# Kernel optimization log

Measured on AMD Instinct MI355X. Metric: run time of the kernel, lower is better.

Reference implementation:

```python
import jax, jax.numpy as jnp
import numpy as np

TS = 1.0  # simulation time step (Ts from network.yaml)


def alpha_psp(x, tau):
    """SLAYER psp: causal temporal conv of x (time-major, (T,...)) with the
    SRM alpha kernel eps[k] = (k*Ts/tau)*exp(1 - k*Ts/tau), scaled by Ts.
    eps[k] = (Ts*e/tau) * k * d**k with d = exp(-Ts/tau), realized exactly by a
    2-state linear recurrence instead of an O(T^2) FIR."""
    d = jnp.asarray(np.exp(-TS / tau), x.dtype)
    c = jnp.asarray(np.e * TS / tau * TS, x.dtype)  # kernel amp * Ts integration

    def step(carry, x_t):
        u, v = carry                       # u = sum x_s d^(t-1-s); v = sum x_s (t-1-s) d^(t-1-s)
        v_new = d * (v + u)                # -> sum_{s<=t} x_s (t-s) d^(t-s)  (x_t weight 0)
        u_new = d * u + x_t
        return (u_new, v_new), c * v_new

    z = jnp.zeros_like(x[0])
    _, out = jax.lax.scan(step, (z, z), x)
    return out


def lif_spike(u_in, theta, tauRef, scaleRef):
    """SLAYER spike function: sequential threshold over time with alpha-shaped
    refractory response nu[k] = -scaleRef*theta*(k*Ts/tauRef)*exp(1-k*Ts/tauRef)
    added after every spike. Same 2-state recurrence generates the refractory
    sum exactly. u_in is time-major (T, ...). Spike amplitude is 1/Ts."""
    d = jnp.asarray(np.exp(-TS / tauRef), u_in.dtype)
    c = jnp.asarray(-scaleRef * theta * np.e * TS / tauRef, u_in.dtype)

    def step(carry, u_t):
        u, v = carry
        v_new = d * (v + u)                # refractory state from past spikes only
        m = u_t + c * v_new                # membrane potential incl. refractory
        s = (m >= theta).astype(u_t.dtype)
        return (d * u + s, v_new), (s / TS, m)

    z = jnp.zeros_like(u_in[0])
    _, (spikes, membrane) = jax.lax.scan(step, (z, z), u_in)
    return spikes, membrane


def conv2d_t(x, w, pad):
    """Per-time-step 2D conv (SLAYER conv3d with time-kernel 1, no bias).
    x: (T, N, C, H, W), w: (O, I, kh, kw)."""
    T, N, C, H, W = x.shape
    y = jax.lax.conv_general_dilated(
        x.reshape(T * N, C, H, W), w, (1, 1), [(pad, pad), (pad, pad)],
        dimension_numbers=('NCHW', 'OIHW', 'NCHW'))
    return y.reshape(T, N, -1, H, W)


def setup_inputs() -> dict:
    key = jax.random.key(0)
    k1, k2, k3 = jax.random.split(key, 3)
    # binary event spike train, (N, C, H, W, T)
    spikeInput = (jax.random.uniform(k1, (4, 1, 192, 192, 64)) < 0.2).astype(jnp.float32)
    # SLAYER conv weights (bias=False); scaled up (weightScale~100 in SLAYER)
    W1 = jax.random.normal(k2, (1, 1, 5, 5), jnp.float32) * 10.0
    W2 = jax.random.normal(k3, (1, 1, 3, 3), jnp.float32) * 10.0
    return {"spikeInput": spikeInput, "W1": W1, "W2": W2}


def reference(spikeInput, W1, W2):
    x = jnp.moveaxis(spikeInput, -1, 0)          # (T, N, C, H, W) time-major
    psp1 = alpha_psp(x, tau=1.0)                 # slayer1.psp (tauSr=1)
    s1, _ = lif_spike(conv2d_t(psp1, W1, 2), theta=30.0, tauRef=1.0, scaleRef=1.0)
    psp2 = alpha_psp(s1, tau=2.0)                # slayer2.psp (tauSr=2)
    s2, _ = lif_spike(conv2d_t(psp2, W2, 1), theta=50.0, tauRef=2.0, scaleRef=1.0)
    return jnp.moveaxis(s2, 0, -1)               # back to (N, C, H, W, T)
```

## Files before the change

### kernel.cpp

```cpp
#include <hip/hip_runtime.h>


#define HH   192
#define WW   192
#define NIMG 4
#define TT   64
#define NT   256
#define XW   6
#define XH   12

#define E_D 2.718281828459045
static constexpr float D1  = (float)0.36787944117144233;
static constexpr float CP1 = (float)(E_D);
static constexpr float DR1 = (float)0.36787944117144233;
static constexpr float CR1 = (float)(-30.0 * E_D);
static constexpr float D2  = (float)0.6065306597126334;
static constexpr float CP2 = (float)(E_D * 0.5);
static constexpr float DR2 = (float)0.6065306597126334;
static constexpr float CR2 = (float)(-50.0 * E_D * 0.5);
static constexpr float TH1 = 30.0f;
static constexpr float TH2 = 50.0f;

__global__ __launch_bounds__(NT)
void ka_pack(const float* __restrict__ in, unsigned* __restrict__ bitT) {
    const int gw = blockIdx.x * (NT / 64) + (threadIdx.x >> 6);
    const int ln = threadIdx.x & 63;
    const int xw = gw % XW;
    const int ny = gw / XW;
    const float* src = in + ((size_t)ny * WW + xw * 32) * TT + ln;
    unsigned w = 0u;
#pragma unroll
    for (int x = 0; x < 32; x++) {
        const float v = src[(size_t)x * TT];
        w |= (v != 0.f) ? (1u << x) : 0u;
    }
    bitT[((size_t)ny * XW + xw) * TT + ln] = w;
}

__global__ __launch_bounds__(NT, 8)
void l1_convscan(const unsigned* __restrict__ bitT, const float* __restrict__ w1g,
                 unsigned short* __restrict__ s1h) {
    __shared__ float ct[64 * 65];
    __shared__ uint2 tb[64];

    const int n = blockIdx.z, ys = blockIdx.y, xs = blockIdx.x;
    const int y0 = ys * 4, x0 = xs * 16;
    const int tid = threadIdx.x;
    const int wv = tid >> 6, ln = tid & 63;

    float w1r[25];
#pragma unroll
    for (int k = 0; k < 25; k++) w1r[k] = w1g[k];

    const int a = (x0 - 2) >> 5;
    const int s = (x0 - 2) & 31;
    const int gyb = y0 + wv;
    unsigned w20[5];
#pragma unroll
    for (int dy = 0; dy < 5; dy++) {
        const int gy = gyb - 2 + dy;
        unsigned wa = 0u, wb = 0u;
        if (gy >= 0 && gy < HH) {
            const unsigned* rp = bitT + ((size_t)(n * HH + gy) * XW) * TT + ln;
            if (a >= 0)     wa = rp[(size_t)a * TT];
            if (a + 1 < XW) wb = rp[(size_t)(a + 1) * TT];
        }
        w20[dy] = (wa >> s) | (wb << (32 - s));
    }

#pragma unroll
    for (int col = 0; col < 16; col++) {
        float l0 = 0.f, l1 = 0.f, l2 = 0.f, l3 = 0.f, l4 = 0.f;
#pragma unroll
        for (int j = 0; j < 5; j++) {
            l0 += (float)((w20[0] >> (col + j)) & 1u) * w1r[j];
            l1 += (float)((w20[1] >> (col + j)) & 1u) * w1r[5 + j];
            l2 += (float)((w20[2] >> (col + j)) & 1u) * w1r[10 + j];
            l3 += (float)((w20[3] >> (col + j)) & 1u) * w1r[15 + j];
            l4 += (float)((w20[4] >> (col + j)) & 1u) * w1r[20 + j];
        }
        ct[(wv * 16 + col) * 65 + ln] = ((l0 + l1) + (l2 + l3)) + l4;
    }
    __syncthreads();

    if (tid < 64) {
        const int px = tid;
        float u1 = 0.f, v1 = 0.f, ur = 0.f, vr = 0.f;
        unsigned slo = 0u, shi = 0u;
#pragma unroll
        for (int tc = 0; tc < TT; tc += 8) {
            float c8[8];
#pragma unroll
            for (int j = 0; j < 8; j++) c8[j] = ct[px * 65 + tc + j];
#pragma unroll
            for (int j = 0; j < 8; j++) {
                v1 = D1 * (v1 + u1);
                const float p = CP1 * v1;
                u1 = D1 * u1 + c8[j];
                vr = DR1 * (vr + ur);
                const float m = p + CR1 * vr;
                const bool sp = (m >= TH1);
                ur = DR1 * ur + (sp ? 1.f : 0.f);
                const unsigned bit = sp ? (1u << ((tc + j) & 31)) : 0u;
                if (tc < 32) slo |= bit;
                else         shi |= bit;
            }
        }
        tb[px] = make_uint2(slo, shi);
    }
    __syncthreads();

    {
        unsigned h = 0u;
#pragma unroll
        for (int x = 0; x < 16; x++) {
            const uint2 b = tb[wv * 16 + x];
            const unsigned w = (ln < 32) ? b.x : b.y;
            h |= ((w >> (ln & 31)) & 1u) << x;
        }
        s1h[((size_t)(n * HH + gyb) * XH + xs) * TT + ln] = (unsigned short)h;
    }
}

__global__ __launch_bounds__(NT, 8)
void l2_convscan(const unsigned short* __restrict__ s1h, const float* __restrict__ w2g,
                 float* __restrict__ out) {
    __shared__ float          lut3[512];
    __shared__ unsigned short ptile[64 * 66];
    __shared__ uint2          tb[64];

    const int n = blockIdx.z, ys = blockIdx.y, xs = blockIdx.x;
    const int y0 = ys * 4;
    const int tid = threadIdx.x;
    const int wv = tid >> 6, ln = tid & 63;

#pragma unroll
    for (int e = tid; e < 512; e += NT) {
        float l0 = 0.f, l1 = 0.f, l2 = 0.f;
#pragma unroll
        for (int j = 0; j < 3; j++) {
            if ((e >> j) & 1)       l0 += w2g[j];
            if ((e >> (3 + j)) & 1) l1 += w2g[3 + j];
            if ((e >> (6 + j)) & 1) l2 += w2g[6 + j];
        }
        lut3[e] = (l0 + l1) + l2;
    }

    const int gyb = y0 + wv;
    unsigned w18[3];
#pragma unroll
    for (int dy = 0; dy < 3; dy++) {
        const int gy = gyb - 1 + dy;
        unsigned hm = 0u, h0 = 0u, hp = 0u;
        if (gy >= 0 && gy < HH) {
            const unsigned short* rp = s1h + ((size_t)(n * HH + gy) * XH) * TT + ln;
            if (xs > 0)      hm = rp[(size_t)(xs - 1) * TT];
            h0 = rp[(size_t)xs * TT];
            if (xs + 1 < XH) hp = rp[(size_t)(xs + 1) * TT];
        }
        w18[dy] = (hm >> 15) | (h0 << 1) | ((hp & 1u) << 17);
    }
    __syncthreads();

#pragma unroll
    for (int col = 0; col < 16; col++) {
        const unsigned pat = ((w18[0] >> col) & 7)
                           | (((w18[1] >> col) & 7) << 3)
                           | (((w18[2] >> col) & 7) << 6);
        ptile[(wv * 16 + col) * 66 + ln] = (unsigned short)pat;
    }
    __syncthreads();

    if (tid < 64) {
        const int px = tid;
        const unsigned* pp = (const unsigned*)(ptile + px * 66);
        float u2 = 0.f, v2 = 0.f, ur2 = 0.f, vr2 = 0.f;
        unsigned olo = 0u, ohi = 0u;
#pragma unroll
        for (int tc = 0; tc < TT; tc += 8) {
            unsigned q[4];
#pragma unroll
            for (int k = 0; k < 4; k++) q[k] = pp[tc / 2 + k];
            float l[8];
#pragma unroll
            for (int k = 0; k < 4; k++) {
                l[2 * k + 0] = lut3[q[k] & 0x1ffu];
                l[2 * k + 1] = lut3[(q[k] >> 16) & 0x1ffu];
            }
#pragma unroll
            for (int j = 0; j < 8; j++) {
                v2 = D2 * (v2 + u2);
                const float p = CP2 * v2;
                u2 = D2 * u2 + l[j];
                vr2 = DR2 * (vr2 + ur2);
                const float m = p + CR2 * vr2;
                const bool sp = (m >= TH2);
                ur2 = DR2 * ur2 + (sp ? 1.f : 0.f);
                const unsigned bit = sp ? (1u << ((tc + j) & 31)) : 0u;
                if (tc < 32) olo |= bit;
                else         ohi |= bit;
            }
        }
        tb[px] = make_uint2(olo, ohi);
    }
    __syncthreads();

    const int sh = ln & 31;
#pragma unroll
    for (int k = 0; k < 16; k++) {
        const uint2 b = tb[wv * 16 + k];
        const unsigned w = (ln < 32) ? b.x : b.y;
        out[((size_t)(n * HH + gyb) * WW + xs * 16 + k) * TT + ln] =
            (float)((w >> sh) & 1u);
    }
}

extern "C" void kernel_launch(void* const* d_in, const int* in_sizes, int n_in,
                              void* d_out, int out_size, void* d_ws, size_t ws_size,
                              hipStream_t stream) {
    const float* in = (const float*)d_in[0];
    const float* w1 = (const float*)d_in[1];
    const float* w2 = (const float*)d_in[2];
    float* out = (float*)d_out;

    char* ws = (char*)d_ws;
    unsigned*       bitT = (unsigned*)ws;
    unsigned short* s1h  = (unsigned short*)(ws + (2ull << 20));

    const int ka_blocks = (NIMG * HH * XW) / (NT / 64);
    dim3 cgrid(WW / 16, HH / 4, NIMG);
    ka_pack    <<<ka_blocks, NT, 0, stream>>>(in, bitT);
    l1_convscan<<<cgrid, NT, 0, stream>>>(bitT, w1, s1h);
    l2_convscan<<<cgrid, NT, 0, stream>>>(s1h, w2, out);
}
```

Measured before the change: 115.1 us.

## Fuse layer-1 and layer-2 conv-scan kernels into one tiled kernel with halo recompute

Merges the two conv+scan kernels into one kernel working on 16x16 output tiles. It recomputes an 18x18 halo of layer-1 spikes in shared memory, so the s1h intermediate no longer round-trips through global memory and one launch is removed. Layer-2 now runs its scan across all 256 threads instead of 64 per block. In exchange it redoes about 27% extra layer-1 work for the halo and uses more shared memory per block (occupancy hint lowered to 4). The layer-1 scan runs in three serial groups of 108 threads, which leaves many lanes idle.

```diff
diff --git a/kernel.cpp b/kernel.cpp
--- a/kernel.cpp
+++ b/kernel.cpp
@@ -7,7 +7,6 @@
 #define TT   64
 #define NT   256
 #define XW   6
-#define XH   12
 
 #define E_D 2.718281828459045
 static constexpr float D1  = (float)0.36787944117144233;
@@ -37,103 +36,26 @@
     bitT[((size_t)ny * XW + xw) * TT + ln] = w;
 }
 
-__global__ __launch_bounds__(NT, 8)
-void l1_convscan(const unsigned* __restrict__ bitT, const float* __restrict__ w1g,
-                 unsigned short* __restrict__ s1h) {
-    __shared__ float ct[64 * 65];
-    __shared__ uint2 tb[64];
-
-    const int n = blockIdx.z, ys = blockIdx.y, xs = blockIdx.x;
-    const int y0 = ys * 4, x0 = xs * 16;
+__global__ __launch_bounds__(NT, 4)
+void lf_fused(const unsigned* __restrict__ bitT, const float* __restrict__ w1g,
+              const float* __restrict__ w2g, float* __restrict__ out) {
+    __shared__ float    ubuf[8448];
+    __shared__ uint2    s1b[18 * 18];
+    __shared__ unsigned wrow[18 * 64];
+    __shared__ uint2    tb[NT];
+    __shared__ float    lut3[512];
+
+    float*          ct    = ubuf;
+    unsigned short* ptile = (unsigned short*)ubuf;
+
+    const int n = blockIdx.z, ty = blockIdx.y, tx = blockIdx.x;
+    const int y0 = ty * 16, x0 = tx * 16;
     const int tid = threadIdx.x;
     const int wv = tid >> 6, ln = tid & 63;
 
     float w1r[25];
 #pragma unroll
     for (int k = 0; k < 25; k++) w1r[k] = w1g[k];
-
-    const int a = (x0 - 2) >> 5;
-    const int s = (x0 - 2) & 31;
-    const int gyb = y0 + wv;
-    unsigned w20[5];
-#pragma unroll
-    for (int dy = 0; dy < 5; dy++) {
-        const int gy = gyb - 2 + dy;
-        unsigned wa = 0u, wb = 0u;
-        if (gy >= 0 && gy < HH) {
-            const unsigned* rp = bitT + ((size_t)(n * HH + gy) * XW) * TT + ln;
-            if (a >= 0)     wa = rp[(size_t)a * TT];
-            if (a + 1 < XW) wb = rp[(size_t)(a + 1) * TT];
-        }
-        w20[dy] = (wa >> s) | (wb << (32 - s));
-    }
-
-#pragma unroll
-    for (int col = 0; col < 16; col++) {
-        float l0 = 0.f, l1 = 0.f, l2 = 0.f, l3 = 0.f, l4 = 0.f;
-#pragma unroll
-        for (int j = 0; j < 5; j++) {
-            l0 += (float)((w20[0] >> (col + j)) & 1u) * w1r[j];
-            l1 += (float)((w20[1] >> (col + j)) & 1u) * w1r[5 + j];
-            l2 += (float)((w20[2] >> (col + j)) & 1u) * w1r[10 + j];
-            l3 += (float)((w20[3] >> (col + j)) & 1u) * w1r[15 + j];
-            l4 += (float)((w20[4] >> (col + j)) & 1u) * w1r[20 + j];
-        }
-        ct[(wv * 16 + col) * 65 + ln] = ((l0 + l1) + (l2 + l3)) + l4;
-    }
-    __syncthreads();
-
-    if (tid < 64) {
-        const int px = tid;
-        float u1 = 0.f, v1 = 0.f, ur = 0.f, vr = 0.f;
-        unsigned slo = 0u, shi = 0u;
-#pragma unroll
-        for (int tc = 0; tc < TT; tc += 8) {
-            float c8[8];
-#pragma unroll
-            for (int j = 0; j < 8; j++) c8[j] = ct[px * 65 + tc + j];
-#pragma unroll
-            for (int j = 0; j < 8; j++) {
-                v1 = D1 * (v1 + u1);
-                const float p = CP1 * v1;
-                u1 = D1 * u1 + c8[j];
-                vr = DR1 * (vr + ur);
-                const float m = p + CR1 * vr;
-                const bool sp = (m >= TH1);
-                ur = DR1 * ur + (sp ? 1.f : 0.f);
-                const unsigned bit = sp ? (1u << ((tc + j) & 31)) : 0u;
-                if (tc < 32) slo |= bit;
-                else         shi |= bit;
-            }
-        }
-        tb[px] = make_uint2(slo, shi);
-    }
-    __syncthreads();
-
-    {
-        unsigned h = 0u;
-#pragma unroll
-        for (int x = 0; x < 16; x++) {
-            const uint2 b = tb[wv * 16 + x];
-            const unsigned w = (ln < 32) ? b.x : b.y;
-            h |= ((w >> (ln & 31)) & 1u) << x;
-        }
-        s1h[((size_t)(n * HH + gyb) * XH + xs) * TT + ln] = (unsigned short)h;
-    }
-}
-
-__global__ __launch_bounds__(NT, 8)
-void l2_convscan(const unsigned short* __restrict__ s1h, const float* __restrict__ w2g,
-                 float* __restrict__ out) {
-    __shared__ float          lut3[512];
-    __shared__ unsigned short ptile[64 * 66];
-    __shared__ uint2          tb[64];
-
-    const int n = blockIdx.z, ys = blockIdx.y, xs = blockIdx.x;
-    const int y0 = ys * 4;
-    const int tid = threadIdx.x;
-    const int wv = tid >> 6, ln = tid & 63;
-
 #pragma unroll
     for (int e = tid; e < 512; e += NT) {
         float l0 = 0.f, l1 = 0.f, l2 = 0.f;
@@ -146,32 +68,108 @@
         lut3[e] = (l0 + l1) + l2;
     }
 
-    const int gyb = y0 + wv;
-    unsigned w18[3];
-#pragma unroll
-    for (int dy = 0; dy < 3; dy++) {
-        const int gy = gyb - 1 + dy;
-        unsigned hm = 0u, h0 = 0u, hp = 0u;
-        if (gy >= 0 && gy < HH) {
-            const unsigned short* rp = s1h + ((size_t)(n * HH + gy) * XH) * TT + ln;
-            if (xs > 0)      hm = rp[(size_t)(xs - 1) * TT];
-            h0 = rp[(size_t)xs * TT];
-            if (xs + 1 < XH) hp = rp[(size_t)(xs + 1) * TT];
-        }
-        w18[dy] = (hm >> 15) | (h0 << 1) | ((hp & 1u) << 17);
+    const int a = (x0 - 3) >> 5;
+    const int s = (x0 - 3) & 31;
+
+#pragma unroll
+    for (int g = 0; g < 3; g++) {
+#pragma unroll
+        for (int pass = 0; pass < 2; pass++) {
+            const int sub = pass * 4 + wv;
+            if (sub < 6) {
+                const int r = g * 6 + sub;
+                const int gy1 = y0 - 1 + r;
+                unsigned w22[5];
+#pragma unroll
+                for (int dy = 0; dy < 5; dy++) {
+                    const int gy = gy1 - 2 + dy;
+                    unsigned wa = 0u, wb = 0u;
+                    if (gy >= 0 && gy < HH) {
+                        const unsigned* rp =
+                            bitT + ((size_t)(n * HH + gy) * XW) * TT + ln;
+                        if (a >= 0)     wa = rp[(size_t)a * TT];
+                        if (a + 1 < XW) wb = rp[(size_t)(a + 1) * TT];
+                    }
+                    w22[dy] = (wa >> s) | (wb << (32 - s));
+                }
+#pragma unroll
+                for (int cc = 0; cc < 18; cc++) {
+                    float l0 = 0.f, l1 = 0.f, l2 = 0.f, l3 = 0.f, l4 = 0.f;
+#pragma unroll
+                    for (int j = 0; j < 5; j++) {
+                        l0 += (float)((w22[0] >> (cc + j)) & 1u) * w1r[j];
+                        l1 += (float)((w22[1] >> (cc + j)) & 1u) * w1r[5 + j];
+                        l2 += (float)((w22[2] >> (cc + j)) & 1u) * w1r[10 + j];
+                        l3 += (float)((w22[3] >> (cc + j)) & 1u) * w1r[15 + j];
+                        l4 += (float)((w22[4] >> (cc + j)) & 1u) * w1r[20 + j];
+                    }
+                    ct[(sub * 18 + cc) * 65 + ln] = ((l0 + l1) + (l2 + l3)) + l4;
+                }
+            }
+        }
+        __syncthreads();
+
+        if (tid < 108) {
+            const int px = tid;
+            const int sub = px / 18, cc = px - sub * 18;
+            const int r = g * 6 + sub;
+            float u1 = 0.f, v1 = 0.f, ur = 0.f, vr = 0.f;
+            unsigned slo = 0u, shi = 0u;
+#pragma unroll
+            for (int tc = 0; tc < TT; tc += 8) {
+                float c8[8];
+#pragma unroll
+                for (int j = 0; j < 8; j++) c8[j] = ct[px * 65 + tc + j];
+#pragma unroll
+                for (int j = 0; j < 8; j++) {
+                    v1 = D1 * (v1 + u1);
+                    const float p = CP1 * v1;
+                    u1 = D1 * u1 + c8[j];
+                    vr = DR1 * (vr + ur);
+                    const float m = p + CR1 * vr;
+                    const bool sp = (m >= TH1);
+                    ur = DR1 * ur + (sp ? 1.f : 0.f);
+                    const unsigned bit = sp ? (1u << ((tc + j) & 31)) : 0u;
+                    if (tc < 32) slo |= bit;
+                    else         shi |= bit;
+                }
+            }
+            const int gy1 = y0 - 1 + r, gx1 = x0 - 1 + cc;
+            const bool valid = (gy1 >= 0 && gy1 < HH && gx1 >= 0 && gx1 < WW);
+            s1b[r * 18 + cc] = make_uint2(valid ? slo : 0u, valid ? shi : 0u);
+        }
+        __syncthreads();
+    }
+
+    for (int r = wv; r < 18; r += 4) {
+        unsigned h = 0u;
+#pragma unroll
+        for (int c = 0; c < 18; c++) {
+            const uint2 b = s1b[r * 18 + c];
+            const unsigned w = (ln < 32) ? b.x : b.y;
+            h |= ((w >> (ln & 31)) & 1u) << c;
+        }
+        wrow[r * 64 + ln] = h;
     }
     __syncthreads();
 
 #pragma unroll
-    for (int col = 0; col < 16; col++) {
-        const unsigned pat = ((w18[0] >> col) & 7)
-                           | (((w18[1] >> col) & 7) << 3)
-                           | (((w18[2] >> col) & 7) << 6);
-        ptile[(wv * 16 + col) * 66 + ln] = (unsigned short)pat;
+    for (int rp = 0; rp < 4; rp++) {
+        const int orow = wv * 4 + rp;
+        const unsigned h0 = wrow[(orow + 0) * 64 + ln];
+        const unsigned h1 = wrow[(orow + 1) * 64 + ln];
+        const unsigned h2 = wrow[(orow + 2) * 64 + ln];
+#pragma unroll
+        for (int oc = 0; oc < 16; oc++) {
+            const unsigned pat = ((h0 >> oc) & 7)
+                               | (((h1 >> oc) & 7) << 3)
+                               | (((h2 >> oc) & 7) << 6);
+            ptile[(orow * 16 + oc) * 66 + ln] = (unsigned short)pat;
+        }
     }
     __syncthreads();
 
-    if (tid < 64) {
+    {
         const int px = tid;
         const unsigned* pp = (const unsigned*)(ptile + px * 66);
         float u2 = 0.f, v2 = 0.f, ur2 = 0.f, vr2 = 0.f;
@@ -207,10 +205,11 @@
 
     const int sh = ln & 31;
 #pragma unroll
-    for (int k = 0; k < 16; k++) {
-        const uint2 b = tb[wv * 16 + k];
+    for (int k = 0; k < 64; k++) {
+        const int p = wv * 64 + k;
+        const uint2 b = tb[p];
         const unsigned w = (ln < 32) ? b.x : b.y;
-        out[((size_t)(n * HH + gyb) * WW + xs * 16 + k) * TT + ln] =
+        out[((size_t)(n * HH + y0 + (p >> 4)) * WW + x0 + (p & 15)) * TT + ln] =
             (float)((w >> sh) & 1u);
     }
 }
@@ -223,13 +222,10 @@
     const float* w2 = (const float*)d_in[2];
     float* out = (float*)d_out;
 
-    char* ws = (char*)d_ws;
-    unsigned*       bitT = (unsigned*)ws;
-    unsigned short* s1h  = (unsigned short*)(ws + (2ull << 20));
+    unsigned* bitT = (unsigned*)d_ws;
 
     const int ka_blocks = (NIMG * HH * XW) / (NT / 64);
-    dim3 cgrid(WW / 16, HH / 4, NIMG);
-    ka_pack    <<<ka_blocks, NT, 0, stream>>>(in, bitT);
-    l1_convscan<<<cgrid, NT, 0, stream>>>(bitT, w1, s1h);
-    l2_convscan<<<cgrid, NT, 0, stream>>>(s1h, w2, out);
+    dim3 fgrid(WW / 16, HH / 16, NIMG);
+    ka_pack <<<ka_blocks, NT, 0, stream>>>(in, bitT);
+    lf_fused<<<fgrid, NT, 0, stream>>>(bitT, w1, w2, out);
 }
```

Measured after the change: 125.7 us. +9.3%, slower.
